# Kernel tuning notes

Measured on AMD Instinct MI355X. Metric: run time of the kernel, lower is better.

Reference implementation:

```python
import jax, jax.numpy as jnp
import numpy as np

# Static config (Swin-T stage 1, SW-MSA)
B = 32; H = 56; W = 56; C = 96; NH = 3; WS = 7; SHIFT = 3
N = WS * WS                 # tokens per window (49)
NW = (H // WS) * (W // WS)  # windows per image (64)
HD = C // NH                # head dim (32)
SCALE = HD ** -0.5
EPS = 1e-3  # keras LayerNormalization default epsilon


def _rel_index():
    # Matches tf.stack(tf.meshgrid(h, w)) with default 'xy' indexing
    xx, yy = np.meshgrid(np.arange(WS), np.arange(WS))
    coords = np.stack([xx, yy]).reshape(2, -1)              # [2, 49]
    rel = (coords[:, :, None] - coords[:, None, :]).transpose(1, 2, 0)
    rel[:, :, 0] += WS - 1
    rel[:, :, 1] += WS - 1
    rel[:, :, 0] *= 2 * WS - 1
    return rel.sum(-1)                                       # [49, 49]

REL_IDX = jnp.asarray(_rel_index())


def _attn_mask():
    # Standard Swin shifted-window attention mask
    img = np.zeros((H, W))
    cnt = 0
    sl = (slice(0, -WS), slice(-WS, -SHIFT), slice(-SHIFT, None))
    for hs in sl:
        for ws_ in sl:
            img[hs, ws_] = cnt
            cnt += 1
    win = img.reshape(H // WS, WS, W // WS, WS).transpose(0, 2, 1, 3).reshape(-1, N)
    diff = win[:, None, :] - win[:, :, None]
    return jnp.asarray(np.where(diff != 0, -100.0, 0.0), dtype=np.float32)  # [nW,49,49]

MASK = _attn_mask()


def _ln(x, g, b):
    mu = x.mean(-1, keepdims=True)
    var = ((x - mu) ** 2).mean(-1, keepdims=True)
    return (x - mu) / jnp.sqrt(var + EPS) * g + b


def setup_inputs() -> dict:
    key = jax.random.key(0)
    ks = jax.random.split(key, 6)
    f32 = jnp.float32
    return {
        "x": jax.random.normal(ks[0], (B, H * W, C), f32),
        "norm1_g": jnp.ones((C,), f32), "norm1_b": jnp.zeros((C,), f32),
        "qkv_w": jax.random.normal(ks[1], (C, 3 * C), f32) * 0.02,
        "qkv_b": jnp.zeros((3 * C,), f32),
        "bias_table": jax.random.normal(ks[2], ((2 * WS - 1) ** 2, NH), f32) * 0.02,
        "proj_w": jax.random.normal(ks[3], (C, C), f32) * 0.02,
        "proj_b": jnp.zeros((C,), f32),
        "norm2_g": jnp.ones((C,), f32), "norm2_b": jnp.zeros((C,), f32),
        "fc1_w": jax.random.normal(ks[4], (C, 4 * C), f32) * 0.02,
        "fc1_b": jnp.zeros((4 * C,), f32),
        "fc2_w": jax.random.normal(ks[5], (4 * C, C), f32) * 0.02,
        "fc2_b": jnp.zeros((C,), f32),
    }


def reference(x, norm1_g, norm1_b, qkv_w, qkv_b, bias_table, proj_w, proj_b,
              norm2_g, norm2_b, fc1_w, fc1_b, fc2_w, fc2_b):
    shortcut = x
    h = _ln(x, norm1_g, norm1_b).reshape(B, H, W, C)
    # cyclic shift (SW-MSA)
    h = jnp.roll(h, (-SHIFT, -SHIFT), axis=(1, 2))
    # window partition -> [B*nW, N, C]
    h = h.reshape(B, H // WS, WS, W // WS, WS, C).transpose(0, 1, 3, 2, 4, 5).reshape(-1, N, C)
    qkv = (h @ qkv_w + qkv_b).reshape(-1, N, 3, NH, HD).transpose(2, 0, 3, 1, 4)
    q, k, v = qkv[0], qkv[1], qkv[2]            # each [B*nW, NH, N, HD]
    attn = jnp.einsum('bhnd,bhmd->bhnm', q * SCALE, k)
    bias = bias_table[REL_IDX.reshape(-1)].reshape(N, N, NH).transpose(2, 0, 1)
    attn = attn + bias[None]
    attn = attn.reshape(B, NW, NH, N, N) + MASK[None, :, None]
    attn = attn.reshape(-1, NH, N, N)
    # NOTE: source applies softmax twice (once in branch, once unconditionally)
    attn = jax.nn.softmax(jax.nn.softmax(attn, axis=-1), axis=-1)
    o = jnp.einsum('bhnm,bhmd->bhnd', attn, v).transpose(0, 2, 1, 3).reshape(-1, N, C)
    o = o @ proj_w + proj_b
    # window reverse + reverse cyclic shift
    o = o.reshape(B, H // WS, W // WS, WS, WS, C).transpose(0, 1, 3, 2, 4, 5).reshape(B, H, W, C)
    o = jnp.roll(o, (SHIFT, SHIFT), axis=(1, 2)).reshape(B, H * W, C)
    x = shortcut + o
    y = _ln(x, norm2_g, norm2_b)
    # NOTE: source Mlp applies gelu in Dense activation AND again in call -> double gelu
    y = jax.nn.gelu(y @ fc1_w + fc1_b, approximate=False)
    y = jax.nn.gelu(y, approximate=False)
    y = y @ fc2_w + fc2_b
    return x + y
```

## Files before the change

kernel.cpp:

```cpp
#include <hip/hip_runtime.h>
#include <math.h>

#define BB   32
#define HH   56
#define WWI  56
#define CC   96
#define NHD  3
#define WSZ  7
#define SHF  3
#define NTK  49
#define NWIN 64
#define HDM  32
#define TOT  (BB*HH*WWI)
#define QKSCALE 0.17677669529663687f
#define LEPS 1e-3f

typedef __attribute__((ext_vector_type(8))) short s8v;
typedef __attribute__((ext_vector_type(4))) float fx4;
typedef unsigned long long ull_t;

#define MFMA16(a,b,c) __builtin_amdgcn_mfma_f32_16x16x32_bf16((a),(b),(c),0,0,0)

__device__ __forceinline__ unsigned short f2bf(float f) {
    union { float f; unsigned u; } v; v.f = f;
    unsigned r = v.u + 0x7FFFu + ((v.u >> 16) & 1u);
    return (unsigned short)(r >> 16);
}

__device__ __forceinline__ float gelu_t(float x) {
    float x2 = x * x;
#if __has_builtin(__builtin_amdgcn_exp2f)
    float z = x * fmaf(-0.10294326f, x2, -2.3022082f);
    float e = __builtin_amdgcn_exp2f(z);
#else
    float z = x * fmaf(-0.07135529f, x2, -1.5957691f);
    float e = __expf(z);
#endif
    return x * __builtin_amdgcn_rcpf(1.f + e);
}

__device__ __forceinline__ int wtok_to_orig(int wt) {
    int win = wt / NTK;
    int p   = wt - win * NTK;
    int b   = win >> 6;
    int w   = win & 63;
    int wi = w >> 3, wj = w & 7;
    int pi = p / WSZ, pj = p - pi * WSZ;
    int r = wi * WSZ + pi + SHF; if (r >= HH) r -= HH;
    int c = wj * WSZ + pj + SHF; if (c >= WWI) c -= WWI;
    return b * (HH * WWI) + r * WWI + c;
}

__device__ __forceinline__ void ln_frag(const float* __restrict__ row,
                                        const float* __restrict__ gg,
                                        const float* __restrict__ bb,
                                        int g4, s8v ha[3])
{
    float h[24];
    #pragma unroll
    for (int ks = 0; ks < 3; ++ks) {
        fx4 v0 = *reinterpret_cast<const fx4*>(row + ks * 32 + g4 * 8);
        fx4 v1 = *reinterpret_cast<const fx4*>(row + ks * 32 + g4 * 8 + 4);
        h[ks*8+0]=v0.x; h[ks*8+1]=v0.y; h[ks*8+2]=v0.z; h[ks*8+3]=v0.w;
        h[ks*8+4]=v1.x; h[ks*8+5]=v1.y; h[ks*8+6]=v1.z; h[ks*8+7]=v1.w;
    }
    float s = 0.f, s2 = 0.f;
    #pragma unroll
    for (int j = 0; j < 24; ++j) { s += h[j]; s2 = fmaf(h[j], h[j], s2); }
    s  += __shfl_xor(s, 16);  s  += __shfl_xor(s, 32);
    s2 += __shfl_xor(s2, 16); s2 += __shfl_xor(s2, 32);
    const float mu = s * (1.f/CC);
    const float rs = rsqrtf(s2 * (1.f/CC) - mu * mu + LEPS);
    #pragma unroll
    for (int ks = 0; ks < 3; ++ks) {
        union { s8v v; unsigned short u[8]; } p;
        #pragma unroll
        for (int j = 0; j < 8; ++j) {
            int c = ks * 32 + g4 * 8 + j;
            p.u[j] = f2bf((h[ks*8+j] - mu) * rs * gg[c] + bb[c]);
        }
        ha[ks] = p.v;
    }
}

extern "C" __global__ void p0_prep(const float* __restrict__ qw, const float* __restrict__ pw,
                                   const float* __restrict__ w1, const float* __restrict__ w2,
                                   const float* __restrict__ btab,
                                   unsigned short* __restrict__ wsw)
{
    int i = blockIdx.x * 256 + threadIdx.x;
    if (i < 27648) {
        int e = i & 7, f = i >> 3;
        int lane = f & 63, fid = f >> 6;
        int ks = fid % 3, t = fid / 3;
        int nt = t % 6, ck = t / 6;
        int n = ck * 96 + nt * 16 + (lane & 15);
        int k = ks * 32 + (lane >> 4) * 8 + e;
        float v = qw[k * 288 + n];
        if (n < 96) v *= QKSCALE;
        wsw[i] = f2bf(v);
    } else if (i < 36864) {
        int j = i - 27648;
        int e = j & 7, f = j >> 3;
        int lane = f & 63, fid = f >> 6;
        int ks = fid % 3, nt = fid / 3;
        int n = nt * 16 + (lane & 15);
        int k = ks * 32 + (lane >> 4) * 8 + e;
        wsw[i] = f2bf(pw[k * 96 + n]);
    } else if (i < 73728) {
        int j = i - 36864;
        int e = j & 7, f = j >> 3;
        int lane = f & 63, fid = f >> 6;
        int ks = fid % 3, t = fid / 3;
        int nt = t & 3, ck = t >> 2;
        int n = ck * 64 + nt * 16 + (lane & 15);
        int k = ks * 32 + (lane >> 4) * 8 + e;
        wsw[i] = f2bf(w1[k * 384 + n]);
    } else if (i < 110592) {
        int j = i - 73728;
        int e = j & 7, f = j >> 3;
        int lane = f & 63, fid = f >> 6;
        int ks = fid & 1, t = fid >> 1;
        int nt = t % 6, ck = t / 6;
        int n = nt * 16 + (lane & 15);
        int k = ck * 64 + ks * 32 + (lane >> 4) * 8 + e;
        wsw[i] = f2bf(w2[k * 96 + n]);
    } else if (i < 159744) {
        float* bmf = (float*)(wsw + 110592);
        int j = i - 110592;
        int r = j & 3, lane = (j >> 2) & 63;
        int fid = j >> 8;
        int mtnt = fid & 15, t = fid >> 4;
        int mt = mtnt >> 2, nt = mtnt & 3;
        int hd = t % 3, cls = t / 3;
        int m = mt * 16 + (lane >> 4) * 4 + r; if (m > 48) m = 48;
        int n = nt * 16 + (lane & 15);
        float val = 0.f;
        if (n < 49) {
            int it = m / 7, jt = m - it * 7;
            int iu = n / 7, ju = n - iu * 7;
            int li  = (cls & 2) ? (it < 4 ? 1 : 2) : 0;
            int lj  = (cls & 1) ? (jt < 4 ? 1 : 2) : 0;
            int lui = (cls & 2) ? (iu < 4 ? 1 : 2) : 0;
            int luj = (cls & 1) ? (ju < 4 ? 1 : 2) : 0;
            int bidx = (jt - ju + 6) * 13 + (it - iu + 6);
            val = btab[bidx * 3 + hd] + ((li*3+lj) == (lui*3+luj) ? 0.f : -100.f);
        }
        bmf[j] = val;
    }
}

extern "C" __global__ void __launch_bounds__(256, 3) k1_qkv(
    const float* __restrict__ x, const float* __restrict__ g1, const float* __restrict__ b1,
    const unsigned short* __restrict__ qwtf, const float* __restrict__ qb,
    unsigned short* __restrict__ qkvb)
{
    const int tid = threadIdx.x, wave = tid >> 6, lane = tid & 63;
    const int l15 = lane & 15, g4 = lane >> 4;
    const int row0 = blockIdx.x * 64 + wave * 16;

    s8v ha[3];
    {
        const int orig = wtok_to_orig(row0 + l15);
        ln_frag(x + (size_t)orig * CC, g1, b1, g4, ha);
    }

    #pragma unroll
    for (int ck = 0; ck < 3; ++ck) {
        fx4 acc[6];
        #pragma unroll
        for (int nt = 0; nt < 6; ++nt) acc[nt] = (fx4){0.f,0.f,0.f,0.f};
        #pragma unroll
        for (int ks = 0; ks < 3; ++ks) {
            #pragma unroll
            for (int nt = 0; nt < 6; ++nt) {
                s8v b = *reinterpret_cast<const s8v*>(
                    &qwtf[(((ck * 6 + nt) * 3 + ks) * 64 + lane) * 8]);
                acc[nt] = MFMA16(ha[ks], b, acc[nt]);
            }
        }
        const int rowb = row0 + g4 * 4;
        const float qmul = (ck == 0) ? QKSCALE : 1.f;
        #pragma unroll
        for (int nt = 0; nt < 6; ++nt) {
            const int col = ck * 96 + nt * 16 + l15;
            const float qbc = qb[col] * qmul;
            #pragma unroll
            for (int r = 0; r < 4; ++r)
                qkvb[(size_t)(rowb + r) * 288 + col] = f2bf(acc[nt][r] + qbc);
        }
    }
}

extern "C" __global__ void __launch_bounds__(64, 3) k2_attn(
    unsigned short* __restrict__ qkvb, const float* __restrict__ bmf)
{
    __shared__ unsigned short P[64][72];
    const int lane = threadIdx.x;
    const int l15 = lane & 15, g4 = lane >> 4;
    const int task = blockIdx.x;
    const int win = task / 3, h = task - win * 3;
    const int g0  = win * NTK;
    const int w   = win & 63;
    const int cls = (((w >> 3) == 7) ? 2 : 0) + (((w & 7) == 7) ? 1 : 0);
    const float* BMF = bmf + (size_t)(cls * 3 + h) * 4096;

    s8v aq[4], bk[4];
    #pragma unroll
    for (int mt = 0; mt < 4; ++mt) {
        int tok = mt * 16 + l15; if (tok > 48) tok = 48;
        const unsigned short* qp = &qkvb[(size_t)(g0 + tok) * 288 + h * HDM + g4 * 8];
        aq[mt] = *reinterpret_cast<const s8v*>(qp);
        bk[mt] = *reinterpret_cast<const s8v*>(qp + 96);
    }

    fx4 sc[4][4];
    #pragma unroll
    for (int mt = 0; mt < 4; ++mt)
        #pragma unroll
        for (int nt = 0; nt < 4; ++nt)
            sc[mt][nt] = MFMA16(aq[mt], bk[nt], ((fx4){0.f,0.f,0.f,0.f}));

    #pragma unroll
    for (int mt = 0; mt < 4; ++mt) {
        fx4 bmv[4];
        #pragma unroll
        for (int nt = 0; nt < 4; ++nt)
            bmv[nt] = *reinterpret_cast<const fx4*>(&BMF[((mt * 4 + nt) << 8) + lane * 4]);
        #pragma unroll
        for (int r = 0; r < 4; ++r) {
            float rs1 = 0.f;
            #pragma unroll
            for (int nt = 0; nt < 4; ++nt) {
                const int n = nt * 16 + l15;
                float s = sc[mt][nt][r] + bmv[nt][r];
                float e = (n < NTK) ? __expf(s) : 0.f;
                sc[mt][nt][r] = e;
                rs1 += e;
            }
            rs1 += __shfl_xor(rs1, 1); rs1 += __shfl_xor(rs1, 2);
            rs1 += __shfl_xor(rs1, 4); rs1 += __shfl_xor(rs1, 8);
            const float iv1 = 1.f / rs1;
            float rs2 = 0.f;
            #pragma unroll
            for (int nt = 0; nt < 4; ++nt) {
                const int n = nt * 16 + l15;
                float e2 = (n < NTK) ? __expf(sc[mt][nt][r] * iv1) : 0.f;
                sc[mt][nt][r] = e2;
                rs2 += e2;
            }
            rs2 += __shfl_xor(rs2, 1); rs2 += __shfl_xor(rs2, 2);
            rs2 += __shfl_xor(rs2, 4); rs2 += __shfl_xor(rs2, 8);
            const float iv2 = 1.f / rs2;
            const int m = mt * 16 + g4 * 4 + r;
            #pragma unroll
            for (int nt = 0; nt < 4; ++nt)
                P[m][nt * 16 + l15] = f2bf(sc[mt][nt][r] * iv2);
        }
    }
    __syncthreads();

    fx4 oc[4][2];
    #pragma unroll
    for (int mt = 0; mt < 4; ++mt) { oc[mt][0] = (fx4){0.f,0.f,0.f,0.f}; oc[mt][1] = (fx4){0.f,0.f,0.f,0.f}; }
    #pragma unroll
    for (int ks = 0; ks < 2; ++ks) {
        s8v vb[2];
        #pragma unroll
        for (int nt = 0; nt < 2; ++nt) {
            union { s8v v; unsigned short u[8]; } pv;
            #pragma unroll
            for (int j = 0; j < 8; ++j) {
                int tok = ks * 32 + g4 * 8 + j; if (tok > 48) tok = 48;
                pv.u[j] = qkvb[(size_t)(g0 + tok) * 288 + 192 + h * HDM + nt * 16 + l15];
            }
            vb[nt] = pv.v;
        }
        #pragma unroll
        for (int mt = 0; mt < 4; ++mt) {
            s8v pa = *reinterpret_cast<const s8v*>(&P[mt * 16 + l15][ks * 32 + g4 * 8]);
            oc[mt][0] = MFMA16(pa, vb[0], oc[mt][0]);
            oc[mt][1] = MFMA16(pa, vb[1], oc[mt][1]);
        }
    }
    #pragma unroll
    for (int mt = 0; mt < 4; ++mt) {
        #pragma unroll
        for (int r = 0; r < 4; ++r) {
            const int m = mt * 16 + g4 * 4 + r;
            if (m < NTK) {
                qkvb[(size_t)(g0 + m) * 288 + h * HDM + l15]      = f2bf(oc[mt][0][r]);
                qkvb[(size_t)(g0 + m) * 288 + h * HDM + 16 + l15] = f2bf(oc[mt][1][r]);
            }
        }
    }
}

extern "C" __global__ void __launch_bounds__(256, 3) k2b_proj(
    const unsigned short* __restrict__ qkvb, const unsigned short* __restrict__ pwtf,
    const float* __restrict__ pb, const float* __restrict__ x, float* __restrict__ out)
{
    const int tid = threadIdx.x, wave = tid >> 6, lane = tid & 63;
    const int l15 = lane & 15, g4 = lane >> 4;
    const int row0 = blockIdx.x * 64 + wave * 16;

    const unsigned short* arow = qkvb + (size_t)(row0 + l15) * 288 + g4 * 8;
    s8v a[3];
    a[0] = *reinterpret_cast<const s8v*>(arow);
    a[1] = *reinterpret_cast<const s8v*>(arow + 32);
    a[2] = *reinterpret_cast<const s8v*>(arow + 64);

    fx4 acc[6];
    #pragma unroll
    for (int nt = 0; nt < 6; ++nt) acc[nt] = (fx4){0.f,0.f,0.f,0.f};
    #pragma unroll
    for (int ks = 0; ks < 3; ++ks) {
        #pragma unroll
        for (int nt = 0; nt < 6; ++nt) {
            s8v b = *reinterpret_cast<const s8v*>(&pwtf[((nt * 3 + ks) * 64 + lane) * 8]);
            acc[nt] = MFMA16(a[ks], b, acc[nt]);
        }
    }
    int orig[4];
    #pragma unroll
    for (int r = 0; r < 4; ++r)
        orig[r] = wtok_to_orig(row0 + g4 * 4 + r);
    #pragma unroll
    for (int nt = 0; nt < 6; ++nt) {
        const int col = nt * 16 + l15;
        const float pbc = pb[col];
        #pragma unroll
        for (int r = 0; r < 4; ++r) {
            const size_t idx = (size_t)orig[r] * CC + col;
            out[idx] = acc[nt][r] + pbc + x[idx];
        }
    }
}

#define LDA 72
extern "C" __global__ void __launch_bounds__(256, 3) k3_mlp(
    float* __restrict__ xio, const float* __restrict__ g2, const float* __restrict__ b2,
    const unsigned short* __restrict__ w1f, const float* __restrict__ bf1,
    const unsigned short* __restrict__ w2f, const float* __restrict__ bf2)
{
    __shared__ unsigned short Ac[64 * LDA];
    const int tid = threadIdx.x, wave = tid >> 6, lane = tid & 63;
    const int l15 = lane & 15, g4 = lane >> 4;
    const int row0 = blockIdx.x * 64 + wave * 16;

    s8v ha[3];
    ln_frag(xio + (size_t)(row0 + l15) * CC, g2, b2, g4, ha);

    fx4 oacc[6];
    #pragma unroll
    for (int nt = 0; nt < 6; ++nt) oacc[nt] = (fx4){0.f,0.f,0.f,0.f};

    #pragma unroll 1
    for (int ck = 0; ck < 6; ++ck) {
        fx4 a1[4];
        #pragma unroll
        for (int nt = 0; nt < 4; ++nt) a1[nt] = (fx4){0.f,0.f,0.f,0.f};
        #pragma unroll
        for (int ks = 0; ks < 3; ++ks) {
            #pragma unroll
            for (int nt = 0; nt < 4; ++nt) {
                s8v b = *reinterpret_cast<const s8v*>(
                    &w1f[(((ck * 4 + nt) * 3 + ks) * 64 + lane) * 8]);
                a1[nt] = MFMA16(ha[ks], b, a1[nt]);
            }
        }
        #pragma unroll
        for (int nt = 0; nt < 4; ++nt) {
            const float bb = bf1[ck * 64 + nt * 16 + l15];
            #pragma unroll
            for (int r = 0; r < 4; ++r) {
                float v0 = a1[nt][r] + bb;
                Ac[(wave*16 + g4*4 + r) * LDA + nt*16 + l15] = f2bf(gelu_t(gelu_t(v0)));
            }
        }
        #pragma unroll
        for (int ks = 0; ks < 2; ++ks) {
            s8v a = *reinterpret_cast<const s8v*>(&Ac[(wave*16 + l15)*LDA + ks*32 + g4*8]);
            #pragma unroll
            for (int nt = 0; nt < 6; ++nt) {
                s8v b = *reinterpret_cast<const s8v*>(
                    &w2f[(((ck * 6 + nt) * 2 + ks) * 64 + lane) * 8]);
                oacc[nt] = MFMA16(a, b, oacc[nt]);
            }
        }
    }

    const int rowb = row0 + g4 * 4;
    #pragma unroll
    for (int nt = 0; nt < 6; ++nt) {
        const int col = nt * 16 + l15;
        const float bb = bf2[col];
        #pragma unroll
        for (int r = 0; r < 4; ++r) {
            const size_t idx = (size_t)(rowb + r) * CC + col;
            xio[idx] = xio[idx] + oacc[nt][r] + bb;
        }
    }
}

extern "C" void kernel_launch(void* const* d_in, const int* in_sizes, int n_in,
                              void* d_out, int out_size, void* d_ws, size_t ws_size,
                              hipStream_t stream)
{
    const float* x    = (const float*)d_in[0];
    const float* n1g  = (const float*)d_in[1];
    const float* n1b  = (const float*)d_in[2];
    const float* qw   = (const float*)d_in[3];
    const float* qb   = (const float*)d_in[4];
    const float* btab = (const float*)d_in[5];
    const float* pw   = (const float*)d_in[6];
    const float* pb   = (const float*)d_in[7];
    const float* n2g  = (const float*)d_in[8];
    const float* n2b  = (const float*)d_in[9];
    const float* w1   = (const float*)d_in[10];
    const float* bf1  = (const float*)d_in[11];
    const float* w2   = (const float*)d_in[12];
    const float* bf2  = (const float*)d_in[13];
    float* out = (float*)d_out;

    unsigned short* qkvb = (unsigned short*)d_ws;
    unsigned short* wbf  = qkvb + (size_t)TOT * 288;
    unsigned short* qwtf = wbf;
    unsigned short* pwtf = qwtf + 27648;
    unsigned short* w1f  = pwtf + 9216;
    unsigned short* w2f  = w1f + 36864;
    float* bmf = (float*)(wbf + 110592);

    p0_prep <<<624, 256, 0, stream>>>(qw, pw, w1, w2, btab, wbf);
    k1_qkv  <<<TOT/64, 256, 0, stream>>>(x, n1g, n1b, qwtf, qb, qkvb);
    k2_attn <<<BB*NWIN*NHD, 64, 0, stream>>>(qkvb, bmf);
    k2b_proj<<<TOT/64, 256, 0, stream>>>(qkvb, pwtf, pb, x, out);
    k3_mlp  <<<TOT/64, 256, 0, stream>>>(out, n2g, n2b, w1f, bf1, w2f, bf2);
}
```

Baseline: 142.6 us.

## Fuse output projection with MLP block, keeping residual rows in shared memory

Merges the projection and MLP kernels into one kernel. Each block now gathers window-ordered attention rows for its 64 original-order tokens, applies the projection plus bias and residual, and stages the result in a shared-memory tile. LayerNorm and the MLP then read from that tile instead of global memory. This removes one launch and a full fp32 write/read round trip of the intermediate activation, at the cost of scattered gathers from qkvb, extra shared memory (about 25KB X2) and possible occupancy loss.

```diff
diff --git a/kernel.cpp b/kernel.cpp
--- a/kernel.cpp
+++ b/kernel.cpp
@@ -296,60 +296,62 @@
     }
 }
 
-extern "C" __global__ void __launch_bounds__(256, 3) k2b_proj(
+#define LDA 72
+#define LDX2 100
+extern "C" __global__ void __launch_bounds__(256, 3) k23_fused(
     const unsigned short* __restrict__ qkvb, const unsigned short* __restrict__ pwtf,
-    const float* __restrict__ pb, const float* __restrict__ x, float* __restrict__ out)
-{
-    const int tid = threadIdx.x, wave = tid >> 6, lane = tid & 63;
-    const int l15 = lane & 15, g4 = lane >> 4;
-    const int row0 = blockIdx.x * 64 + wave * 16;
-
-    const unsigned short* arow = qkvb + (size_t)(row0 + l15) * 288 + g4 * 8;
-    s8v a[3];
-    a[0] = *reinterpret_cast<const s8v*>(arow);
-    a[1] = *reinterpret_cast<const s8v*>(arow + 32);
-    a[2] = *reinterpret_cast<const s8v*>(arow + 64);
-
-    fx4 acc[6];
-    #pragma unroll
-    for (int nt = 0; nt < 6; ++nt) acc[nt] = (fx4){0.f,0.f,0.f,0.f};
-    #pragma unroll
-    for (int ks = 0; ks < 3; ++ks) {
-        #pragma unroll
-        for (int nt = 0; nt < 6; ++nt) {
-            s8v b = *reinterpret_cast<const s8v*>(&pwtf[((nt * 3 + ks) * 64 + lane) * 8]);
-            acc[nt] = MFMA16(a[ks], b, acc[nt]);
-        }
-    }
-    int orig[4];
-    #pragma unroll
-    for (int r = 0; r < 4; ++r)
-        orig[r] = wtok_to_orig(row0 + g4 * 4 + r);
-    #pragma unroll
-    for (int nt = 0; nt < 6; ++nt) {
-        const int col = nt * 16 + l15;
-        const float pbc = pb[col];
-        #pragma unroll
-        for (int r = 0; r < 4; ++r) {
-            const size_t idx = (size_t)orig[r] * CC + col;
-            out[idx] = acc[nt][r] + pbc + x[idx];
-        }
-    }
-}
-
-#define LDA 72
-extern "C" __global__ void __launch_bounds__(256, 3) k3_mlp(
-    float* __restrict__ xio, const float* __restrict__ g2, const float* __restrict__ b2,
+    const float* __restrict__ pb, const float* __restrict__ x,
+    const float* __restrict__ g2, const float* __restrict__ b2,
     const unsigned short* __restrict__ w1f, const float* __restrict__ bf1,
-    const unsigned short* __restrict__ w2f, const float* __restrict__ bf2)
-{
+    const unsigned short* __restrict__ w2f, const float* __restrict__ bf2,
+    float* __restrict__ out)
+{
+    __shared__ float X2[64][LDX2];
     __shared__ unsigned short Ac[64 * LDA];
     const int tid = threadIdx.x, wave = tid >> 6, lane = tid & 63;
     const int l15 = lane & 15, g4 = lane >> 4;
     const int row0 = blockIdx.x * 64 + wave * 16;
 
+    s8v a[3];
+    {
+        const int t = row0 + l15;
+        const int b = t / (HH * WWI), rc = t - b * (HH * WWI);
+        const int orr = rc / WWI, occ = rc - orr * WWI;
+        int wr = orr + (HH - SHF); if (wr >= HH) wr -= HH;
+        int wc = occ + (WWI - SHF); if (wc >= WWI) wc -= WWI;
+        const int wtok = (b * 64 + (wr / WSZ) * 8 + (wc / WSZ)) * NTK
+                         + (wr % WSZ) * WSZ + (wc % WSZ);
+        const unsigned short* arow = qkvb + (size_t)wtok * 288 + g4 * 8;
+        a[0] = *reinterpret_cast<const s8v*>(arow);
+        a[1] = *reinterpret_cast<const s8v*>(arow + 32);
+        a[2] = *reinterpret_cast<const s8v*>(arow + 64);
+    }
+    {
+        fx4 acc[6];
+        #pragma unroll
+        for (int nt = 0; nt < 6; ++nt) acc[nt] = (fx4){0.f,0.f,0.f,0.f};
+        #pragma unroll
+        for (int ks = 0; ks < 3; ++ks) {
+            #pragma unroll
+            for (int nt = 0; nt < 6; ++nt) {
+                s8v b = *reinterpret_cast<const s8v*>(&pwtf[((nt * 3 + ks) * 64 + lane) * 8]);
+                acc[nt] = MFMA16(a[ks], b, acc[nt]);
+            }
+        }
+        #pragma unroll
+        for (int nt = 0; nt < 6; ++nt) {
+            const int col = nt * 16 + l15;
+            const float pbc = pb[col];
+            #pragma unroll
+            for (int r = 0; r < 4; ++r) {
+                const int tr = row0 + g4 * 4 + r;
+                X2[wave * 16 + g4 * 4 + r][col] = acc[nt][r] + pbc + x[(size_t)tr * CC + col];
+            }
+        }
+    }
+
     s8v ha[3];
-    ln_frag(xio + (size_t)(row0 + l15) * CC, g2, b2, g4, ha);
+    ln_frag(&X2[wave * 16 + l15][0], g2, b2, g4, ha);
 
     fx4 oacc[6];
     #pragma unroll
@@ -380,12 +382,12 @@
         }
         #pragma unroll
         for (int ks = 0; ks < 2; ++ks) {
-            s8v a = *reinterpret_cast<const s8v*>(&Ac[(wave*16 + l15)*LDA + ks*32 + g4*8]);
+            s8v aa = *reinterpret_cast<const s8v*>(&Ac[(wave*16 + l15)*LDA + ks*32 + g4*8]);
             #pragma unroll
             for (int nt = 0; nt < 6; ++nt) {
                 s8v b = *reinterpret_cast<const s8v*>(
                     &w2f[(((ck * 6 + nt) * 2 + ks) * 64 + lane) * 8]);
-                oacc[nt] = MFMA16(a, b, oacc[nt]);
+                oacc[nt] = MFMA16(aa, b, oacc[nt]);
             }
         }
     }
@@ -397,8 +399,8 @@
         const float bb = bf2[col];
         #pragma unroll
         for (int r = 0; r < 4; ++r) {
-            const size_t idx = (size_t)(rowb + r) * CC + col;
-            xio[idx] = xio[idx] + oacc[nt][r] + bb;
+            out[(size_t)(rowb + r) * CC + col] =
+                X2[wave * 16 + g4 * 4 + r][col] + oacc[nt][r] + bb;
         }
     }
 }
@@ -431,9 +433,9 @@
     unsigned short* w2f  = w1f + 36864;
     float* bmf = (float*)(wbf + 110592);
 
-    p0_prep <<<624, 256, 0, stream>>>(qw, pw, w1, w2, btab, wbf);
-    k1_qkv  <<<TOT/64, 256, 0, stream>>>(x, n1g, n1b, qwtf, qb, qkvb);
-    k2_attn <<<BB*NWIN*NHD, 64, 0, stream>>>(qkvb, bmf);
-    k2b_proj<<<TOT/64, 256, 0, stream>>>(qkvb, pwtf, pb, x, out);
-    k3_mlp  <<<TOT/64, 256, 0, stream>>>(out, n2g, n2b, w1f, bf1, w2f, bf2);
-}
+    p0_prep  <<<624, 256, 0, stream>>>(qw, pw, w1, w2, btab, wbf);
+    k1_qkv   <<<TOT/64, 256, 0, stream>>>(x, n1g, n1b, qwtf, qb, qkvb);
+    k2_attn  <<<BB*NWIN*NHD, 64, 0, stream>>>(qkvb, bmf);
+    k23_fused<<<TOT/64, 256, 0, stream>>>(qkvb, pwtf, pb, x, n2g, n2b,
+                                          w1f, bf1, w2f, bf2, out);
+}
```

Result: faster. 126.7 us (-11.2%).
